# Kernel optimization log

Measured on AMD Instinct MI355X. Metric: run time of the kernel, lower is better.

## Reference

```python
import jax, jax.numpy as jnp
import numpy as np

DIM, NH, HD = 1536, 12, 128
C = HD // 2            # 64 complex (half) dims per head
BANDS = (C - 2 * (C // 3), C // 3, C // 3)   # (22, 21, 21) for T/H/W
EPS = 1e-6
F, Hg, Wg = 6, 20, 32
S = F * Hg * Wg
MAX_LEN = 1024


def _rope_tables(max_len=MAX_LEN):
    # Wan-style 1D rope params per band, concatenated along channel dim -> [max_len, 64]
    pos = np.arange(max_len, dtype=np.float64)
    cos_l, sin_l = [], []
    for bd in BANDS:
        inv = 1.0 / (10000.0 ** (np.arange(bd, dtype=np.float64) / bd))
        ang = np.outer(pos, inv)
        cos_l.append(np.cos(ang))
        sin_l.append(np.sin(ang))
    return (np.concatenate(cos_l, 1).astype(np.float32),
            np.concatenate(sin_l, 1).astype(np.float32))


def setup_inputs() -> dict:
    key = jax.random.key(0)
    ks = jax.random.split(key, 8)
    std = 0.02
    fc, fs = _rope_tables()
    return {
        "x": jax.random.normal(ks[0], (1, S, DIM), jnp.float32),
        "Wq": jax.random.normal(ks[1], (DIM, DIM), jnp.float32) * std,
        "bq": jnp.zeros((DIM,), jnp.float32),
        "Wk": jax.random.normal(ks[2], (DIM, DIM), jnp.float32) * std,
        "bk": jnp.zeros((DIM,), jnp.float32),
        "Wv": jax.random.normal(ks[3], (DIM, DIM), jnp.float32) * std,
        "bv": jnp.zeros((DIM,), jnp.float32),
        "Wo": jax.random.normal(ks[4], (DIM, DIM), jnp.float32) * std,
        "bo": jnp.zeros((DIM,), jnp.float32),
        "gq": jnp.ones((DIM,), jnp.float32),
        "gk": jnp.ones((DIM,), jnp.float32),
        "freqs_cos": jnp.asarray(fc),
        "freqs_sin": jnp.asarray(fs),
        "f": F, "h": Hg, "w": Wg,
    }


def _rmsnorm(t, g):
    t = t.astype(jnp.float32)
    return t * jax.lax.rsqrt(jnp.mean(t * t, axis=-1, keepdims=True) + EPS) * g


def _grid_freqs(tab, f, h, w):
    # tab: [max_len, 64] -> [f*h*w, 64] via T/H/W band broadcast (mirrors torch expand+cat)
    o1, o2 = BANDS[0], BANDS[0] + BANDS[1]
    t = jnp.broadcast_to(tab[:f, None, None, :o1], (f, h, w, BANDS[0]))
    hh = jnp.broadcast_to(tab[None, :h, None, o1:o2], (f, h, w, BANDS[1]))
    ww = jnp.broadcast_to(tab[None, None, :w, o2:C], (f, h, w, BANDS[2]))
    return jnp.concatenate([t, hh, ww], axis=-1).reshape(f * h * w, 1, C)


def _rope_apply(t, fc, fs):
    # t: [B, S, n, d]; complex mul (a+ib)*(cos+isin) on pairs of channels
    B, Sl, n, d = t.shape
    tr = t.astype(jnp.float32).reshape(B, Sl, n, C, 2)
    a, b = tr[..., 0], tr[..., 1]
    fc = fc[None]  # [1, S, 1, C]
    fs = fs[None]
    out_r = a * fc - b * fs
    out_i = a * fs + b * fc
    return jnp.stack([out_r, out_i], axis=-1).reshape(B, Sl, n, d)


def reference(x, Wq, bq, Wk, bk, Wv, bv, Wo, bo, gq, gk, freqs_cos, freqs_sin, f, h, w):
    B, Sl, _ = x.shape
    q = _rmsnorm(x @ Wq.T + bq, gq).reshape(B, Sl, NH, HD)
    k = _rmsnorm(x @ Wk.T + bk, gk).reshape(B, Sl, NH, HD)
    v = (x @ Wv.T + bv).reshape(B, Sl, NH, HD)

    fc = _grid_freqs(freqs_cos, f, h, w)
    fs = _grid_freqs(freqs_sin, f, h, w)
    q = _rope_apply(q, fc, fs)
    k = _rope_apply(k, fc, fs)

    scale = 1.0 / jnp.sqrt(jnp.float32(HD))
    scores = jnp.einsum('bqnd,bknd->bnqk', q, k) * scale
    p = jax.nn.softmax(scores, axis=-1)
    o = jnp.einsum('bnqk,bknd->bqnd', p, v.astype(jnp.float32))
    o = o.reshape(B, Sl, DIM)
    return o @ Wo.T + bo
```

## Files before the change

### kernel.cpp

```cpp
#include <hip/hip_runtime.h>
#include <hip/hip_bf16.h>
#include <cstdint>

#define DIM 1536
#define NHEADS 12
#define HD 128
#define SEQ 3840

typedef float f32x4 __attribute__((ext_vector_type(4)));
typedef __bf16 bf16x8 __attribute__((ext_vector_type(8)));
typedef __bf16 bf16x4 __attribute__((ext_vector_type(4)));
typedef __bf16 bf16x2 __attribute__((ext_vector_type(2)));
typedef unsigned int u32;
typedef u32 u32x4 __attribute__((ext_vector_type(4)));

#define GLLD(g, l) __builtin_amdgcn_global_load_lds( \
    (const __attribute__((address_space(1))) void*)(g), \
    (__attribute__((address_space(3))) void*)(l), 16, 0, 0)

__global__ __launch_bounds__(256) void cvt_bf16_5(
    const float* __restrict__ s0, const float* __restrict__ s1, const float* __restrict__ s2,
    const float* __restrict__ s3, const float* __restrict__ s4,
    __bf16* __restrict__ d0, __bf16* __restrict__ d1, __bf16* __restrict__ d2,
    __bf16* __restrict__ d3, __bf16* __restrict__ d4,
    int n4_0, int n4_w) {
    const float* src; __bf16* dst; int n4;
    switch (blockIdx.y) {
        case 0: src = s0; dst = d0; n4 = n4_0; break;
        case 1: src = s1; dst = d1; n4 = n4_w; break;
        case 2: src = s2; dst = d2; n4 = n4_w; break;
        case 3: src = s3; dst = d3; n4 = n4_w; break;
        default: src = s4; dst = d4; n4 = n4_w; break;
    }
    int i = blockIdx.x * 256 + threadIdx.x;
    if (i < n4) {
        f32x4 v = ((const f32x4*)src)[i];
        bf16x4 o;
        o[0] = (__bf16)v[0]; o[1] = (__bf16)v[1];
        o[2] = (__bf16)v[2]; o[3] = (__bf16)v[3];
        ((bf16x4*)dst)[i] = o;
    }
}

template <int OUTF32>
__global__ __launch_bounds__(256) void gemm_bt(
    const __bf16* __restrict__ A,
    const __bf16* __restrict__ B0, const __bf16* __restrict__ B1, const __bf16* __restrict__ B2,
    const float* __restrict__ bias0, const float* __restrict__ bias1, const float* __restrict__ bias2,
    void* __restrict__ C0v, void* __restrict__ C1v, void* __restrict__ C2v,
    int N, int K) {
    const __bf16* B = B0; const float* bias = bias0; void* Cv = C0v;
    if (blockIdx.z == 1) { B = B1; bias = bias1; Cv = C1v; }
    else if (blockIdx.z == 2) { B = B2; bias = bias2; Cv = C2v; }

    __shared__ __bf16 As[2][128 * 32];
    __shared__ __bf16 Bs[2][128 * 32];

    const int t = threadIdx.x;
    const int w = t >> 6;
    const int lane = t & 63;
    const int lr = lane & 15, lg = lane >> 4;
    const int wr = (w >> 1) * 64, wc = (w & 1) * 64;
    const int wb = w * 512;

    const long long rowA = (long long)blockIdx.y * 128 + (t >> 2);
    const long long rowB = (long long)blockIdx.x * 128 + (t >> 2);
    const int kcol = (t & 3) * 8;

    const __bf16* pa0 = A + rowA * K + kcol;
    const __bf16* pa1 = pa0 + 64LL * K;
    const __bf16* pb0 = B + rowB * K + kcol;
    const __bf16* pb1 = pb0 + 64LL * K;

    f32x4 acc[4][4] = {};

    auto stage = [&](int kk, int b) {
        GLLD(pa0 + kk, &As[b][wb]);
        GLLD(pa1 + kk, &As[b][2048 + wb]);
        GLLD(pb0 + kk, &Bs[b][wb]);
        GLLD(pb1 + kk, &Bs[b][2048 + wb]);
    };

    stage(0, 0);
    int buf = 0;
#pragma unroll 1
    for (int kk = 0; kk < K; kk += 32) {
        __syncthreads();
        if (kk + 32 < K) stage(kk + 32, buf ^ 1);
        bf16x8 af[4], bfr[4];
#pragma unroll
        for (int m = 0; m < 4; m++)
            af[m] = *(const bf16x8*)(&As[buf][(wr + m * 16 + lr) * 32 + lg * 8]);
#pragma unroll
        for (int n = 0; n < 4; n++)
            bfr[n] = *(const bf16x8*)(&Bs[buf][(wc + n * 16 + lr) * 32 + lg * 8]);
#pragma unroll
        for (int m = 0; m < 4; m++)
#pragma unroll
            for (int n = 0; n < 4; n++)
                acc[m][n] = __builtin_amdgcn_mfma_f32_16x16x32_bf16(af[m], bfr[n], acc[m][n], 0, 0, 0);
        buf ^= 1;
    }

    const int cb = blockIdx.x * 128 + wc;
    const int rb_ = blockIdx.y * 128 + wr;
#pragma unroll
    for (int n = 0; n < 4; n++) {
        int col = cb + n * 16 + lr;
        float bv = bias[col];
#pragma unroll
        for (int m = 0; m < 4; m++) {
            int row0 = rb_ + m * 16 + lg * 4;
#pragma unroll
            for (int r = 0; r < 4; r++) {
                float v = acc[m][n][r] + bv;
                if (OUTF32) ((float*)Cv)[(long long)(row0 + r) * N + col] = v;
                else ((__bf16*)Cv)[(long long)(row0 + r) * N + col] = (__bf16)v;
            }
        }
    }
}

__global__ __launch_bounds__(256) void norm_rope(
    const __bf16* __restrict__ pre,
    const float* __restrict__ gvec,
    const float* __restrict__ fcos,
    const float* __restrict__ fsin,
    __bf16* __restrict__ out) {
    const int s = blockIdx.x;
    const int t = threadIdx.x;
    float a[3], b[3];
    float ss = 0.f;
#pragma unroll
    for (int j = 0; j < 3; j++) {
        int p = t + 256 * j;
        bf16x2 v = *(const bf16x2*)(pre + (size_t)s * DIM + 2 * p);
        a[j] = (float)v[0]; b[j] = (float)v[1];
        ss += a[j] * a[j] + b[j] * b[j];
    }
    for (int off = 32; off; off >>= 1) ss += __shfl_down(ss, off);
    __shared__ float red[4];
    if ((t & 63) == 0) red[t >> 6] = ss;
    __syncthreads();
    float mean = (red[0] + red[1] + red[2] + red[3]) * (1.f / DIM);
    float rms = rsqrtf(mean + 1e-6f);
    const int fi = s / 640, hi2 = (s % 640) >> 5, wi = s & 31;
#pragma unroll
    for (int j = 0; j < 3; j++) {
        int p = t + 256 * j;
        int c = p & 63;
        int pos = (c < 22) ? fi : ((c < 43) ? hi2 : wi);
        float fc = fcos[pos * 64 + c];
        float fs = fsin[pos * 64 + c];
        float av = a[j] * rms * gvec[2 * p];
        float bv = b[j] * rms * gvec[2 * p + 1];
        float orr = av * fc - bv * fs;
        float oi = av * fs + bv * fc;
        int hh = p >> 6;
        bf16x2 o; o[0] = (__bf16)orr; o[1] = (__bf16)oi;
        *(bf16x2*)(out + ((size_t)hh * SEQ + s) * HD + 2 * c) = o;
    }
}

__global__ __launch_bounds__(256) void transpose_bf16(
    const __bf16* __restrict__ in, __bf16* __restrict__ out) {
    __shared__ __bf16 tile[64][68];
    const int t = threadIdx.x;
    const int sb = blockIdx.x * 64, cb = blockIdx.y * 64;
    const int tx = t & 15, ty = t >> 4;
#pragma unroll
    for (int i = 0; i < 4; i++) {
        int r = ty + i * 16;
        bf16x4 v = *(const bf16x4*)(in + (size_t)(sb + r) * DIM + cb + tx * 4);
        *(bf16x4*)&tile[r][tx * 4] = v;
    }
    __syncthreads();
    int s0 = sb + tx * 4;
    int j = (s0 >> 2) & 7;
    int u = (j < 4) ? (j << 1) : ((j << 1) - 7);
    int sp = (s0 & ~31) + (u << 2);
#pragma unroll
    for (int i = 0; i < 4; i++) {
        int c = ty + i * 16;
        bf16x4 v;
        v[0] = tile[tx * 4 + 0][c]; v[1] = tile[tx * 4 + 1][c];
        v[2] = tile[tx * 4 + 2][c]; v[3] = tile[tx * 4 + 3][c];
        *(bf16x4*)(out + (size_t)(cb + c) * SEQ + sp) = v;
    }
}

__global__ __launch_bounds__(384, 1) void attn(
    const __bf16* __restrict__ Q,
    const __bf16* __restrict__ Kk,
    const __bf16* __restrict__ Vp,
    __bf16* __restrict__ O) {
    __shared__ __bf16 Ks[2][64 * 128];
    __shared__ __bf16 Vs[2][128 * 64];

    const int bid = blockIdx.x;
    const int task = (bid & 7) * 30 + (bid >> 3);
    const int h = task / 20;
    const int qb = task % 20;
    const int t = threadIdx.x;
    const int wv = t >> 6;
    const int lane = t & 63;
    const int lq = lane & 15, g = lane >> 4;
    const int q0 = qb * 192 + wv * 32;

    const __bf16* Qh = Q + (size_t)h * SEQ * HD;
    const __bf16* Kh = Kk + (size_t)h * SEQ * HD;
    const __bf16* Vh = Vp + (size_t)h * HD * SEQ;

    bf16x8 qf[2][4];
#pragma unroll
    for (int qg = 0; qg < 2; qg++)
#pragma unroll
        for (int c = 0; c < 4; c++)
            qf[qg][c] = *(const bf16x8*)(Qh + (size_t)(q0 + qg * 16 + lq) * HD + c * 32 + g * 8);

    f32x4 acc[8][2] = {};
    float m[2] = {-1e30f, -1e30f}, l[2] = {0.f, 0.f};
    const float SCL2 = 0.1275365308119098f;
    const float THR_RAW = 90.50966799187809f;

    const int krow_in = lane >> 4;
    const int vrow_in = lane >> 3;
    const int vce = (((lane & 7) ^ (lane >> 3))) * 8;
    auto stage = [&](int kv0, int b) {
        for (int c = wv; c < 32; c += 6) {
            if (c < 16) {
                int r = c * 4 + krow_in;
                int cb = ((lane & 15) * 16) ^ ((r & 7) << 4);
                GLLD(Kh + (size_t)(kv0 + r) * HD + (cb >> 1), &Ks[b][c * 512]);
            } else {
                int cc = c - 16;
                int rd = cc * 8 + vrow_in;
                GLLD(Vh + (size_t)rd * SEQ + kv0 + vce, &Vs[b][cc * 512]);
            }
        }
    };

    stage(0, 0);
    int buf = 0;
    const int kswz = (lq & 7) << 3;
#pragma unroll 1
    for (int i = 0; i < 60; i++) {
        __syncthreads();
        if (i + 1 < 60) stage((i + 1) * 64, buf ^ 1);
        const __bf16* Kb_ = &Ks[buf][0];
        const __bf16* Vb_ = &Vs[buf][0];

#pragma unroll
        for (int s = 0; s < 2; s++) {
            f32x4 sc[2][2] = {};
            __builtin_amdgcn_s_setprio(1);
#pragma unroll
            for (int c = 0; c < 4; c++) {
                int cb = (c * 32 + g * 8) ^ kswz;
                bf16x8 k0 = *(const bf16x8*)(Kb_ + (s * 32 + lq) * 128 + cb);
                bf16x8 k1 = *(const bf16x8*)(Kb_ + (s * 32 + 16 + lq) * 128 + cb);
                sc[0][0] = __builtin_amdgcn_mfma_f32_16x16x32_bf16(k0, qf[0][c], sc[0][0], 0, 0, 0);
                sc[0][1] = __builtin_amdgcn_mfma_f32_16x16x32_bf16(k0, qf[1][c], sc[0][1], 0, 0, 0);
                sc[1][0] = __builtin_amdgcn_mfma_f32_16x16x32_bf16(k1, qf[0][c], sc[1][0], 0, 0, 0);
                sc[1][1] = __builtin_amdgcn_mfma_f32_16x16x32_bf16(k1, qf[1][c], sc[1][1], 0, 0, 0);
            }
            __builtin_amdgcn_s_setprio(0);

            bf16x8 pa[2];
#pragma unroll
            for (int qg = 0; qg < 2; qg++) {
                float pm = fmaxf(fmaxf(fmaxf(sc[0][qg][0], sc[0][qg][1]), fmaxf(sc[0][qg][2], sc[0][qg][3])),
                                 fmaxf(fmaxf(sc[1][qg][0], sc[1][qg][1]), fmaxf(sc[1][qg][2], sc[1][qg][3])));
                pm = fmaxf(pm, __shfl_xor(pm, 16));
                pm = fmaxf(pm, __shfl_xor(pm, 32));
                if (!__all(pm <= m[qg] + THR_RAW)) {
                    float mn = fmaxf(m[qg], pm);
                    float al = __builtin_amdgcn_exp2f(SCL2 * (m[qg] - mn));
                    m[qg] = mn;
                    l[qg] *= al;
#pragma unroll
                    for (int dt = 0; dt < 8; dt++)
#pragma unroll
                        for (int r = 0; r < 4; r++) acc[dt][qg][r] *= al;
                }
                float ms = SCL2 * m[qg];
                float p[8], ls = 0.f;
#pragma unroll
                for (int r = 0; r < 4; r++) { p[r] = __builtin_amdgcn_exp2f(SCL2 * sc[0][qg][r] - ms); ls += p[r]; }
#pragma unroll
                for (int r = 0; r < 4; r++) { p[4 + r] = __builtin_amdgcn_exp2f(SCL2 * sc[1][qg][r] - ms); ls += p[4 + r]; }
                ls += __shfl_xor(ls, 16);
                ls += __shfl_xor(ls, 32);
                l[qg] += ls;
#pragma unroll
                for (int i2 = 0; i2 < 8; i2++) pa[qg][i2] = (__bf16)p[i2];
            }

            bf16x8 vf[8];
#pragma unroll
            for (int dt = 0; dt < 8; dt++)
                vf[dt] = *(const bf16x8*)(Vb_ + (dt * 16 + lq) * 64 + ((s * 32 + g * 8) ^ kswz));
            __builtin_amdgcn_s_setprio(1);
#pragma unroll
            for (int dt = 0; dt < 8; dt++) {
                acc[dt][0] = __builtin_amdgcn_mfma_f32_16x16x32_bf16(vf[dt], pa[0], acc[dt][0], 0, 0, 0);
                acc[dt][1] = __builtin_amdgcn_mfma_f32_16x16x32_bf16(vf[dt], pa[1], acc[dt][1], 0, 0, 0);
            }
            __builtin_amdgcn_s_setprio(0);
        }
        buf ^= 1;
    }

#pragma unroll
    for (int qg = 0; qg < 2; qg++) {
        float inv = 1.f / l[qg];
#pragma unroll
        for (int dt = 0; dt < 8; dt++) {
            bf16x4 o;
#pragma unroll
            for (int r = 0; r < 4; r++) o[r] = (__bf16)(acc[dt][qg][r] * inv);
            *(bf16x4*)(O + (size_t)(q0 + qg * 16 + lq) * DIM + h * HD + dt * 16 + g * 4) = o;
        }
    }
}

extern "C" void kernel_launch(void* const* d_in, const int* in_sizes, int n_in,
                              void* d_out, int out_size, void* d_ws, size_t ws_size,
                              hipStream_t stream) {
    const float* x = (const float*)d_in[0];
    const float* Wq = (const float*)d_in[1];
    const float* bq = (const float*)d_in[2];
    const float* Wk = (const float*)d_in[3];
    const float* bk = (const float*)d_in[4];
    const float* Wv = (const float*)d_in[5];
    const float* bv = (const float*)d_in[6];
    const float* Wo = (const float*)d_in[7];
    const float* bo = (const float*)d_in[8];
    const float* gq = (const float*)d_in[9];
    const float* gk = (const float*)d_in[10];
    const float* fcos = (const float*)d_in[11];
    const float* fsin = (const float*)d_in[12];
    float* out = (float*)d_out;

    char* ws = (char*)d_ws;
    const size_t SZ_SD = (size_t)SEQ * DIM * 2;
    const size_t SZ_W = (size_t)DIM * DIM * 2;
    __bf16* xb   = (__bf16*)ws;            ws += SZ_SD;
    __bf16* Wqb  = (__bf16*)ws;            ws += SZ_W;
    __bf16* Wkb  = (__bf16*)ws;            ws += SZ_W;
    __bf16* Wvb  = (__bf16*)ws;            ws += SZ_W;
    __bf16* Wob  = (__bf16*)ws;            ws += SZ_W;
    __bf16* qpre = (__bf16*)ws;            ws += SZ_SD;
    __bf16* kpre = (__bf16*)ws;            ws += SZ_SD;
    __bf16* vpre = (__bf16*)ws;            ws += SZ_SD;
    __bf16* Kb   = (__bf16*)ws;            ws += SZ_SD;
    __bf16* Vtb  = (__bf16*)ws;            ws += SZ_SD;
    __bf16* Qb = xb;
    __bf16* ob = qpre;

    const int n4_x = SEQ * DIM / 4;
    const int n4_w = DIM * DIM / 4;
    cvt_bf16_5<<<dim3((n4_x + 255) / 256, 5), 256, 0, stream>>>(
        x, Wq, Wk, Wv, Wo, xb, Wqb, Wkb, Wvb, Wob, n4_x, n4_w);

    gemm_bt<0><<<dim3(DIM / 128, SEQ / 128, 3), 256, 0, stream>>>(
        xb, Wqb, Wkb, Wvb, bq, bk, bv, qpre, kpre, vpre, DIM, DIM);

    norm_rope<<<SEQ, 256, 0, stream>>>(qpre, gq, fcos, fsin, Qb);
    norm_rope<<<SEQ, 256, 0, stream>>>(kpre, gk, fcos, fsin, Kb);
    transpose_bf16<<<dim3(SEQ / 64, DIM / 64), 256, 0, stream>>>(vpre, Vtb);

    attn<<<dim3(240), 384, 0, stream>>>(Qb, Kb, Vtb, ob);

    gemm_bt<1><<<dim3(DIM / 128, SEQ / 128, 1), 256, 0, stream>>>(
        ob, Wob, Wob, Wob, bo, bo, bo, out, out, out, DIM, DIM);
}
```

Baseline: 320.8 us.

## Split attention KV range across two blocks with a merge kernel

```diff
diff --git a/kernel.cpp b/kernel.cpp
--- a/kernel.cpp
+++ b/kernel.cpp
@@ -6,6 +6,8 @@
 #define NHEADS 12
 #define HD 128
 #define SEQ 3840
+#define SCL2F 0.1275365308119098f
+#define THRRAW 90.50966799187809f
 
 typedef float f32x4 __attribute__((ext_vector_type(4)));
 typedef __bf16 bf16x8 __attribute__((ext_vector_type(8)));
@@ -121,12 +123,14 @@
     }
 }
 
-__global__ __launch_bounds__(256) void norm_rope(
-    const __bf16* __restrict__ pre,
-    const float* __restrict__ gvec,
-    const float* __restrict__ fcos,
-    const float* __restrict__ fsin,
-    __bf16* __restrict__ out) {
+__global__ __launch_bounds__(256) void norm_rope2(
+    const __bf16* __restrict__ qpre, const __bf16* __restrict__ kpre,
+    const float* __restrict__ gq, const float* __restrict__ gk,
+    const float* __restrict__ fcos, const float* __restrict__ fsin,
+    __bf16* __restrict__ Qb, __bf16* __restrict__ Kb) {
+    const __bf16* pre = blockIdx.y ? kpre : qpre;
+    const float* gvec = blockIdx.y ? gk : gq;
+    __bf16* out = blockIdx.y ? Kb : Qb;
     const int s = blockIdx.x;
     const int t = threadIdx.x;
     float a[3], b[3];
@@ -189,23 +193,27 @@
     }
 }
 
-__global__ __launch_bounds__(384, 1) void attn(
+__global__ __launch_bounds__(384, 3) void attn_split(
     const __bf16* __restrict__ Q,
     const __bf16* __restrict__ Kk,
     const __bf16* __restrict__ Vp,
-    __bf16* __restrict__ O) {
+    float* __restrict__ pacc,
+    float2* __restrict__ pml) {
     __shared__ __bf16 Ks[2][64 * 128];
     __shared__ __bf16 Vs[2][128 * 64];
 
     const int bid = blockIdx.x;
-    const int task = (bid & 7) * 30 + (bid >> 3);
-    const int h = task / 20;
-    const int qb = task % 20;
+    const int task = (bid & 7) * 60 + (bid >> 3);
+    const int half = task & 1;
+    const int hq = task >> 1;
+    const int h = hq / 20;
+    const int qb = hq % 20;
     const int t = threadIdx.x;
     const int wv = t >> 6;
     const int lane = t & 63;
     const int lq = lane & 15, g = lane >> 4;
     const int q0 = qb * 192 + wv * 32;
+    const int kvbase = half * (SEQ / 2);
 
     const __bf16* Qh = Q + (size_t)h * SEQ * HD;
     const __bf16* Kh = Kk + (size_t)h * SEQ * HD;
@@ -219,9 +227,8 @@
             qf[qg][c] = *(const bf16x8*)(Qh + (size_t)(q0 + qg * 16 + lq) * HD + c * 32 + g * 8);
 
     f32x4 acc[8][2] = {};
-    float m[2] = {-1e30f, -1e30f}, l[2] = {0.f, 0.f};
-    const float SCL2 = 0.1275365308119098f;
-    const float THR_RAW = 90.50966799187809f;
+    float m[2] = {-1e30f, -1e30f};
+    float lp[2] = {0.f, 0.f};
 
     const int krow_in = lane >> 4;
     const int vrow_in = lane >> 3;
@@ -240,6 +247,147 @@
         }
     };
 
+    stage(kvbase, 0);
+    int buf = 0;
+    const int kswz = (lq & 7) << 3;
+#pragma unroll 1
+    for (int i = 0; i < 30; i++) {
+        __syncthreads();
+        if (i + 1 < 30) stage(kvbase + (i + 1) * 64, buf ^ 1);
+        const __bf16* Kb_ = &Ks[buf][0];
+        const __bf16* Vb_ = &Vs[buf][0];
+
+#pragma unroll
+        for (int s = 0; s < 2; s++) {
+            f32x4 sc[2][2] = {};
+            __builtin_amdgcn_s_setprio(1);
+#pragma unroll
+            for (int c = 0; c < 4; c++) {
+                int cb = (c * 32 + g * 8) ^ kswz;
+                bf16x8 k0 = *(const bf16x8*)(Kb_ + (s * 32 + lq) * 128 + cb);
+                bf16x8 k1 = *(const bf16x8*)(Kb_ + (s * 32 + 16 + lq) * 128 + cb);
+                sc[0][0] = __builtin_amdgcn_mfma_f32_16x16x32_bf16(k0, qf[0][c], sc[0][0], 0, 0, 0);
+                sc[0][1] = __builtin_amdgcn_mfma_f32_16x16x32_bf16(k0, qf[1][c], sc[0][1], 0, 0, 0);
+                sc[1][0] = __builtin_amdgcn_mfma_f32_16x16x32_bf16(k1, qf[0][c], sc[1][0], 0, 0, 0);
+                sc[1][1] = __builtin_amdgcn_mfma_f32_16x16x32_bf16(k1, qf[1][c], sc[1][1], 0, 0, 0);
+            }
+            __builtin_amdgcn_s_setprio(0);
+
+            bf16x8 vf[8];
+#pragma unroll
+            for (int dt = 0; dt < 8; dt++)
+                vf[dt] = *(const bf16x8*)(Vb_ + (dt * 16 + lq) * 64 + ((s * 32 + g * 8) ^ kswz));
+
+            bf16x8 pa[2];
+#pragma unroll
+            for (int qg = 0; qg < 2; qg++) {
+                float pm = fmaxf(fmaxf(fmaxf(sc[0][qg][0], sc[0][qg][1]), fmaxf(sc[0][qg][2], sc[0][qg][3])),
+                                 fmaxf(fmaxf(sc[1][qg][0], sc[1][qg][1]), fmaxf(sc[1][qg][2], sc[1][qg][3])));
+                if (!__all(pm <= m[qg] + THRRAW)) {
+                    pm = fmaxf(pm, __shfl_xor(pm, 16));
+                    pm = fmaxf(pm, __shfl_xor(pm, 32));
+                    float mn = fmaxf(m[qg], pm);
+                    float al = __builtin_amdgcn_exp2f(SCL2F * (m[qg] - mn));
+                    m[qg] = mn;
+                    lp[qg] *= al;
+#pragma unroll
+                    for (int dt = 0; dt < 8; dt++)
+#pragma unroll
+                        for (int r = 0; r < 4; r++) acc[dt][qg][r] *= al;
+                }
+                float ms = SCL2F * m[qg];
+                float p[8], ls = 0.f;
+#pragma unroll
+                for (int r = 0; r < 4; r++) { p[r] = __builtin_amdgcn_exp2f(SCL2F * sc[0][qg][r] - ms); ls += p[r]; }
+#pragma unroll
+                for (int r = 0; r < 4; r++) { p[4 + r] = __builtin_amdgcn_exp2f(SCL2F * sc[1][qg][r] - ms); ls += p[4 + r]; }
+                lp[qg] += ls;
+#pragma unroll
+                for (int i2 = 0; i2 < 8; i2++) pa[qg][i2] = (__bf16)p[i2];
+            }
+
+            __builtin_amdgcn_s_setprio(1);
+#pragma unroll
+            for (int dt = 0; dt < 8; dt++) {
+                acc[dt][0] = __builtin_amdgcn_mfma_f32_16x16x32_bf16(vf[dt], pa[0], acc[dt][0], 0, 0, 0);
+                acc[dt][1] = __builtin_amdgcn_mfma_f32_16x16x32_bf16(vf[dt], pa[1], acc[dt][1], 0, 0, 0);
+            }
+            __builtin_amdgcn_s_setprio(0);
+        }
+        buf ^= 1;
+    }
+
+#pragma unroll
+    for (int qg = 0; qg < 2; qg++) {
+        float lps = lp[qg];
+        lps += __shfl_xor(lps, 16);
+        lps += __shfl_xor(lps, 32);
+        const size_t qrow = (size_t)(half * NHEADS + h) * SEQ + q0 + qg * 16 + lq;
+        if (g == 0) pml[qrow] = float2{m[qg], lps};
+#pragma unroll
+        for (int dt = 0; dt < 8; dt++)
+            *(f32x4*)(pacc + qrow * HD + dt * 16 + g * 4) = acc[dt][qg];
+    }
+}
+
+__global__ __launch_bounds__(256) void attn_merge(
+    const float* __restrict__ pacc, const float2* __restrict__ pml,
+    __bf16* __restrict__ ob) {
+    const int t = threadIdx.x;
+    const int qq = blockIdx.x * 2 + (t >> 7);
+    const int d = t & 127;
+    float2 a = pml[qq], b = pml[NHEADS * SEQ + qq];
+    float M = fmaxf(a.x, b.x);
+    float w0 = __builtin_amdgcn_exp2f(SCL2F * (a.x - M));
+    float w1 = __builtin_amdgcn_exp2f(SCL2F * (b.x - M));
+    float num = pacc[(size_t)qq * HD + d] * w0 +
+                pacc[((size_t)NHEADS * SEQ + qq) * HD + d] * w1;
+    float den = a.y * w0 + b.y * w1;
+    int h = qq / SEQ, s = qq % SEQ;
+    ob[(size_t)s * DIM + h * HD + d] = (__bf16)(num / den);
+}
+
+__global__ __launch_bounds__(384, 1) void attn_single(
+    const __bf16* __restrict__ Q, const __bf16* __restrict__ Kk,
+    const __bf16* __restrict__ Vp, __bf16* __restrict__ O) {
+    __shared__ __bf16 Ks[2][64 * 128];
+    __shared__ __bf16 Vs[2][128 * 64];
+    const int bid = blockIdx.x;
+    const int task = (bid & 7) * 30 + (bid >> 3);
+    const int h = task / 20;
+    const int qb = task % 20;
+    const int t = threadIdx.x;
+    const int wv = t >> 6;
+    const int lane = t & 63;
+    const int lq = lane & 15, g = lane >> 4;
+    const int q0 = qb * 192 + wv * 32;
+    const __bf16* Qh = Q + (size_t)h * SEQ * HD;
+    const __bf16* Kh = Kk + (size_t)h * SEQ * HD;
+    const __bf16* Vh = Vp + (size_t)h * HD * SEQ;
+    bf16x8 qf[2][4];
+#pragma unroll
+    for (int qg = 0; qg < 2; qg++)
+#pragma unroll
+        for (int c = 0; c < 4; c++)
+            qf[qg][c] = *(const bf16x8*)(Qh + (size_t)(q0 + qg * 16 + lq) * HD + c * 32 + g * 8);
+    f32x4 acc[8][2] = {};
+    float m[2] = {-1e30f, -1e30f}, l[2] = {0.f, 0.f};
+    const int krow_in = lane >> 4;
+    const int vrow_in = lane >> 3;
+    const int vce = (((lane & 7) ^ (lane >> 3))) * 8;
+    auto stage = [&](int kv0, int b) {
+        for (int c = wv; c < 32; c += 6) {
+            if (c < 16) {
+                int r = c * 4 + krow_in;
+                int cb = ((lane & 15) * 16) ^ ((r & 7) << 4);
+                GLLD(Kh + (size_t)(kv0 + r) * HD + (cb >> 1), &Ks[b][c * 512]);
+            } else {
+                int cc = c - 16;
+                int rd = cc * 8 + vrow_in;
+                GLLD(Vh + (size_t)rd * SEQ + kv0 + vce, &Vs[b][cc * 512]);
+            }
+        }
+    };
     stage(0, 0);
     int buf = 0;
     const int kswz = (lq & 7) << 3;
@@ -249,11 +397,9 @@
         if (i + 1 < 60) stage((i + 1) * 64, buf ^ 1);
         const __bf16* Kb_ = &Ks[buf][0];
         const __bf16* Vb_ = &Vs[buf][0];
-
 #pragma unroll
         for (int s = 0; s < 2; s++) {
             f32x4 sc[2][2] = {};
-            __builtin_amdgcn_s_setprio(1);
 #pragma unroll
             for (int c = 0; c < 4; c++) {
                 int cb = (c * 32 + g * 8) ^ kswz;
@@ -264,8 +410,6 @@
                 sc[1][0] = __builtin_amdgcn_mfma_f32_16x16x32_bf16(k1, qf[0][c], sc[1][0], 0, 0, 0);
                 sc[1][1] = __builtin_amdgcn_mfma_f32_16x16x32_bf16(k1, qf[1][c], sc[1][1], 0, 0, 0);
             }
-            __builtin_amdgcn_s_setprio(0);
-
             bf16x8 pa[2];
 #pragma unroll
             for (int qg = 0; qg < 2; qg++) {
@@ -273,44 +417,39 @@
                                  fmaxf(fmaxf(sc[1][qg][0], sc[1][qg][1]), fmaxf(sc[1][qg][2], sc[1][qg][3])));
                 pm = fmaxf(pm, __shfl_xor(pm, 16));
                 pm = fmaxf(pm, __shfl_xor(pm, 32));
-                if (!__all(pm <= m[qg] + THR_RAW)) {
+                if (!__all(pm <= m[qg] + THRRAW)) {
                     float mn = fmaxf(m[qg], pm);
-                    float al = __builtin_amdgcn_exp2f(SCL2 * (m[qg] - mn));
-                    m[qg] = mn;
-                    l[qg] *= al;
+                    float al = __builtin_amdgcn_exp2f(SCL2F * (m[qg] - mn));
+                    m[qg] = mn; l[qg] *= al;
 #pragma unroll
                     for (int dt = 0; dt < 8; dt++)
 #pragma unroll
                         for (int r = 0; r < 4; r++) acc[dt][qg][r] *= al;
                 }
-                float ms = SCL2 * m[qg];
+                float ms = SCL2F * m[qg];
                 float p[8], ls = 0.f;
 #pragma unroll
-                for (int r = 0; r < 4; r++) { p[r] = __builtin_amdgcn_exp2f(SCL2 * sc[0][qg][r] - ms); ls += p[r]; }
-#pragma unroll
-                for (int r = 0; r < 4; r++) { p[4 + r] = __builtin_amdgcn_exp2f(SCL2 * sc[1][qg][r] - ms); ls += p[4 + r]; }
+                for (int r = 0; r < 4; r++) { p[r] = __builtin_amdgcn_exp2f(SCL2F * sc[0][qg][r] - ms); ls += p[r]; }
+#pragma unroll
+                for (int r = 0; r < 4; r++) { p[4 + r] = __builtin_amdgcn_exp2f(SCL2F * sc[1][qg][r] - ms); ls += p[4 + r]; }
                 ls += __shfl_xor(ls, 16);
                 ls += __shfl_xor(ls, 32);
                 l[qg] += ls;
 #pragma unroll
                 for (int i2 = 0; i2 < 8; i2++) pa[qg][i2] = (__bf16)p[i2];
             }
-
             bf16x8 vf[8];
 #pragma unroll
             for (int dt = 0; dt < 8; dt++)
                 vf[dt] = *(const bf16x8*)(Vb_ + (dt * 16 + lq) * 64 + ((s * 32 + g * 8) ^ kswz));
-            __builtin_amdgcn_s_setprio(1);
 #pragma unroll
             for (int dt = 0; dt < 8; dt++) {
                 acc[dt][0] = __builtin_amdgcn_mfma_f32_16x16x32_bf16(vf[dt], pa[0], acc[dt][0], 0, 0, 0);
                 acc[dt][1] = __builtin_amdgcn_mfma_f32_16x16x32_bf16(vf[dt], pa[1], acc[dt][1], 0, 0, 0);
             }
-            __builtin_amdgcn_s_setprio(0);
         }
         buf ^= 1;
     }
-
 #pragma unroll
     for (int qg = 0; qg < 2; qg++) {
         float inv = 1.f / l[qg];
@@ -342,21 +481,23 @@
     const float* fsin = (const float*)d_in[12];
     float* out = (float*)d_out;
 
-    char* ws = (char*)d_ws;
+    char* p = (char*)d_ws;
     const size_t SZ_SD = (size_t)SEQ * DIM * 2;
     const size_t SZ_W = (size_t)DIM * DIM * 2;
-    __bf16* xb   = (__bf16*)ws;            ws += SZ_SD;
-    __bf16* Wqb  = (__bf16*)ws;            ws += SZ_W;
-    __bf16* Wkb  = (__bf16*)ws;            ws += SZ_W;
-    __bf16* Wvb  = (__bf16*)ws;            ws += SZ_W;
-    __bf16* Wob  = (__bf16*)ws;            ws += SZ_W;
-    __bf16* qpre = (__bf16*)ws;            ws += SZ_SD;
-    __bf16* kpre = (__bf16*)ws;            ws += SZ_SD;
-    __bf16* vpre = (__bf16*)ws;            ws += SZ_SD;
-    __bf16* Kb   = (__bf16*)ws;            ws += SZ_SD;
-    __bf16* Vtb  = (__bf16*)ws;            ws += SZ_SD;
+    __bf16* xb   = (__bf16*)p;  p += SZ_SD;
+    __bf16* Wob  = (__bf16*)p;  p += SZ_W;
+    __bf16* Wqb  = (__bf16*)p;  p += SZ_W;
+    __bf16* Wkb  = (__bf16*)p;  p += SZ_W;
+    __bf16* Wvb  = (__bf16*)p;  p += SZ_W;
+    __bf16* qpre = (__bf16*)p;  p += SZ_SD;
+    __bf16* kpre = (__bf16*)p;  p += SZ_SD;
+    __bf16* vpre = (__bf16*)p;  p += SZ_SD;
+    __bf16* Kb   = (__bf16*)p;  p += SZ_SD;
+    __bf16* Vtb  = (__bf16*)p;  p += SZ_SD;
+    float2* pml  = (float2*)p;  p += sizeof(float2) * 2 * NHEADS * SEQ;
+    float* pacc = (float*)Wqb;
     __bf16* Qb = xb;
-    __bf16* ob = qpre;
+    const bool split_ok = ws_size >= (size_t)(p - (char*)d_ws);
 
     const int n4_x = SEQ * DIM / 4;
     const int n4_w = DIM * DIM / 4;
@@ -366,12 +507,19 @@
     gemm_bt<0><<<dim3(DIM / 128, SEQ / 128, 3), 256, 0, stream>>>(
         xb, Wqb, Wkb, Wvb, bq, bk, bv, qpre, kpre, vpre, DIM, DIM);
 
-    norm_rope<<<SEQ, 256, 0, stream>>>(qpre, gq, fcos, fsin, Qb);
-    norm_rope<<<SEQ, 256, 0, stream>>>(kpre, gk, fcos, fsin, Kb);
+    norm_rope2<<<dim3(SEQ, 2), 256, 0, stream>>>(qpre, kpre, gq, gk, fcos, fsin, Qb, Kb);
     transpose_bf16<<<dim3(SEQ / 64, DIM / 64), 256, 0, stream>>>(vpre, Vtb);
 
-    attn<<<dim3(240), 384, 0, stream>>>(Qb, Kb, Vtb, ob);
-
-    gemm_bt<1><<<dim3(DIM / 128, SEQ / 128, 1), 256, 0, stream>>>(
-        ob, Wob, Wob, Wob, bo, bo, bo, out, out, out, DIM, DIM);
-}
+    if (split_ok) {
+        __bf16* ob = Kb;
+        attn_split<<<dim3(480), 384, 0, stream>>>(Qb, Kb, Vtb, pacc, pml);
+        attn_merge<<<dim3(NHEADS * SEQ / 2), 256, 0, stream>>>(pacc, pml, ob);
+        gemm_bt<1><<<dim3(DIM / 128, SEQ / 128, 1), 256, 0, stream>>>(
+            ob, Wob, Wob, Wob, bo, bo, bo, out, out, out, DIM, DIM);
+    } else {
+        __bf16* ob = qpre;
+        attn_single<<<dim3(240), 384, 0, stream>>>(Qb, Kb, Vtb, ob);
+        gemm_bt<1><<<dim3(DIM / 128, SEQ / 128, 1), 256, 0, stream>>>(
+            ob, Wob, Wob, Wob, bo, bo, bo, out, out, out, DIM, DIM);
+    }
+}
```

Result: slower. 364.6 us (+13.7%).
